# Kernel optimization log

Hardware: AMD Instinct MI355X
Metric: run time of the kernel (lower is better)

## Reference

```python
import jax, jax.numpy as jnp
import numpy as np

B, C, H, W, K = 16, 64, 256, 256, 3

def setup_inputs() -> dict:
    key = jax.random.key(0)
    ks = jax.random.split(key, 3)
    x = jax.random.normal(ks[0], (B, C, H, W), dtype=jnp.float32)
    # ReDistribution params
    rd_k = jnp.ones((1, C, 1, 1), jnp.float32)
    rd_b = jnp.zeros((1, C, 1, 1), jnp.float32)
    # Spectral binary activation beta
    beta = jnp.ones((1,), jnp.float32)
    # HardBinaryConv real-valued latent weights (Conv2d default init scale)
    fan_in = C * K * K
    bound = 1.0 / np.sqrt(fan_in)
    conv_w = jax.random.uniform(ks[1], (C, C, K, K), jnp.float32, -bound, bound)
    # RPReLU params
    pr_bias0 = jnp.zeros((1, C, 1, 1), jnp.float32)
    prelu_w = jnp.full((C,), 0.25, jnp.float32)
    pr_bias1 = jnp.zeros((1, C, 1, 1), jnp.float32)
    return {"x": x, "rd_k": rd_k, "rd_b": rd_b, "beta": beta,
            "conv_w": conv_w, "pr_bias0": pr_bias0, "prelu_w": prelu_w,
            "pr_bias1": pr_bias1}

def _ste(hard, soft):
    # straight-through estimator: forward=hard, backward grads flow via soft
    return jax.lax.stop_gradient(hard - soft) + soft

def reference(x, rd_k, rd_b, beta, conv_w, pr_bias0, prelu_w, pr_bias1):
    sg = jax.lax.stop_gradient
    # ReDistribution
    out = x * rd_k + rd_b
    # Spectral binary activation with tanh STE
    out = _ste(jnp.sign(out), jnp.tanh(out * beta))
    # HardBinaryConv: per-output-channel mean |w| scaling, sign binarize, clip STE
    scaling = sg(jnp.mean(jnp.abs(conv_w), axis=(1, 2, 3), keepdims=True))  # [C,1,1,1]
    bw = _ste(scaling * jnp.sign(conv_w), jnp.clip(conv_w, -1.0, 1.0))
    y = jax.lax.conv_general_dilated(
        out, bw, window_strides=(1, 1), padding=((1, 1), (1, 1)),
        dimension_numbers=("NCHW", "OIHW", "NCHW"))
    # RPReLU: bias0 -> per-channel PReLU -> bias1
    y = y + pr_bias0
    y = jnp.where(y >= 0, y, prelu_w[None, :, None, None] * y)
    y = y + pr_bias1
    return y + x
```

## Files before the change

kernel.cpp:

```cpp
#include <hip/hip_runtime.h>
#include <cstdint>
#include <cstddef>

#define Bn 16
#define Cn 64
#define Hn 256
#define Wn 256
#define HWn (Hn * Wn)
#define TH 8
#define ROWS (TH + 2)
#define COLS (Wn + 2)
#define NBLK (Bn * (Hn / TH))

typedef unsigned long long u64;
typedef u64   u64x2 __attribute__((ext_vector_type(2)));
typedef float f32x4 __attribute__((ext_vector_type(4)));

__global__ __launch_bounds__(64) void pack_weights(const float* __restrict__ w,
                                                   const float* __restrict__ b0g,
                                                   const float* __restrict__ pwg,
                                                   const float* __restrict__ b1g,
                                                   u64* __restrict__ wbits,
                                                   float4* __restrict__ par,
                                                   int* __restrict__ corrx) {
    const int co = blockIdx.x;
    const int ci = threadIdx.x;
    const float* wp = w + ((size_t)co * Cn + ci) * 9;
    float v[9];
    float asum = 0.f;
    #pragma unroll
    for (int t = 0; t < 9; ++t) { v[t] = wp[t]; asum += fabsf(v[t]); }
    u64 m[9];
    #pragma unroll
    for (int t = 0; t < 9; ++t) m[t] = __ballot(v[t] > 0.f);
    #pragma unroll
    for (int off = 32; off; off >>= 1) asum += __shfl_xor(asum, off);
    if (ci == 0) {
        int c[9];
        #pragma unroll
        for (int t = 0; t < 9; ++t) {
            wbits[co * 9 + t] = m[t];
            c[t] = 64 - 2 * (int)__popcll(m[t]);
        }
        int* cx = corrx + co * 8;
        cx[0] = c[0] + c[1] + c[2];
        cx[1] = c[6] + c[7] + c[8];
        cx[2] = c[0] + c[3] + c[6];
        cx[3] = c[2] + c[5] + c[8];
        cx[4] = c[0]; cx[5] = c[2];
        cx[6] = c[6]; cx[7] = c[8];
        par[co] = make_float4(asum * (1.f / (Cn * 9)), b0g[co], pwg[co], b1g[co]);
    }
}

__global__ __launch_bounds__(256, 3) void fused(const float* __restrict__ x,
                                                const float* __restrict__ rdk,
                                                const float* __restrict__ rdb,
                                                const u64* __restrict__ wbits,
                                                const float4* __restrict__ par,
                                                const int* __restrict__ corrx,
                                                float* __restrict__ out,
                                                int clobber) {
    __shared__ __align__(16) u64 s_a[ROWS][COLS];
    __shared__ float2 s_rd[Cn];

    const int tid = threadIdx.x;
    const int bid     = blockIdx.x;
    const int logical = (bid & 7) * (NBLK / 8) + (bid >> 3);
    const int n  = logical >> 5;
    const int h0 = (logical & 31) * TH;

    if (tid < Cn) s_rd[tid] = make_float2(rdk[tid], rdb[tid]);
    if (tid < 2 * ROWS) s_a[tid >> 1][(tid & 1) ? (COLS - 1) : 0] = 0;
    __syncthreads();

    const float* xn = x + (size_t)n * Cn * HWn;
    #pragma unroll
    for (int it = 0; it < 5; ++it) {
        const int task = tid + it * 256;
        const int r  = task >> 7;
        const int c  = (task & 127) * 2;
        const int gh = h0 - 1 + r;
        u64 b0 = 0, b1 = 0;
        if (gh >= 0 && gh < Hn) {
            const float* xp = xn + (size_t)gh * Wn + c;
            #pragma unroll 8
            for (int ci = 0; ci < Cn; ++ci) {
                const float2 kb = s_rd[ci];
                const float2 v = *reinterpret_cast<const float2*>(xp + (size_t)ci * HWn);
                const u64 bit = 1ull << ci;
                if (fmaf(v.x, kb.x, kb.y) > 0.f) b0 |= bit;
                if (fmaf(v.y, kb.x, kb.y) > 0.f) b1 |= bit;
            }
        }
        s_a[r][1 + c] = b0;
        s_a[r][2 + c] = b1;
    }
    __syncthreads();

    const int r  = tid >> 5;
    const int c0 = (tid & 31) * 8;

    u64 A[3][10];
    #pragma unroll
    for (int dh = 0; dh < 3; ++dh)
        #pragma unroll
        for (int q = 0; q < 5; ++q) {
            const u64x2 t = *reinterpret_cast<const u64x2*>(&s_a[r + dh][c0 + 2 * q]);
            A[dh][2 * q]     = t.x;
            A[dh][2 * q + 1] = t.y;
        }
    if (clobber) s_a[0][tid] = 0;

    const int htop = (h0 == 0) & (r == 0);
    const int hbot = (h0 + TH == Hn) & (r == TH - 1);
    const int wl = (c0 == 0), wr = (c0 == Wn - 8);
    const int need = htop | hbot | wl | wr;
    const int h = h0 + r;

    const float* xp = x   + (size_t)n * Cn * HWn + (size_t)h * Wn + c0;
    float*       op = out + (size_t)n * Cn * HWn + (size_t)h * Wn + c0;

    f32x4 xa = *reinterpret_cast<const f32x4*>(xp);
    f32x4 xb = *reinterpret_cast<const f32x4*>(xp + 4);
    #pragma unroll 2
    for (int co = 0; co < Cn; ++co) {
        const int nco = (co < Cn - 1) ? co + 1 : co;
        const f32x4 xa_n = *reinterpret_cast<const f32x4*>(xp + (size_t)nco * HWn);
        const f32x4 xb_n = *reinterpret_cast<const f32x4*>(xp + (size_t)nco * HWn + 4);

        const u64* wb = wbits + co * 9;
        int isum[8];
        #pragma unroll
        for (int p = 0; p < 8; ++p) {
            int acc = 0;
            #pragma unroll
            for (int dh = 0; dh < 3; ++dh) {
                acc += (int)__popcll(A[dh][p]     ^ wb[dh * 3]);
                acc += (int)__popcll(A[dh][p + 1] ^ wb[dh * 3 + 1]);
                acc += (int)__popcll(A[dh][p + 2] ^ wb[dh * 3 + 2]);
            }
            isum[p] = 576 - 2 * acc;
        }

        if (need) {
            const int* cx = corrx + co * 8;
            const int sb = (htop ? cx[0] : 0) + (hbot ? cx[1] : 0);
            #pragma unroll
            for (int p = 0; p < 8; ++p) isum[p] -= sb;
            if (wl) isum[0] -= cx[2] - (htop ? cx[4] : 0) - (hbot ? cx[6] : 0);
            if (wr) isum[7] -= cx[3] - (htop ? cx[5] : 0) - (hbot ? cx[7] : 0);
        }

        const float4 p4 = par[co];
        f32x4 o0, o1;
        #pragma unroll
        for (int j = 0; j < 4; ++j) {
            float y = fmaf(p4.x, (float)isum[j], p4.y);
            y = (y >= 0.f) ? y : y * p4.z;
            o0[j] = y + p4.w + xa[j];
        }
        #pragma unroll
        for (int j = 0; j < 4; ++j) {
            float y = fmaf(p4.x, (float)isum[4 + j], p4.y);
            y = (y >= 0.f) ? y : y * p4.z;
            o1[j] = y + p4.w + xb[j];
        }
        __builtin_nontemporal_store(o0, reinterpret_cast<f32x4*>(op + (size_t)co * HWn));
        __builtin_nontemporal_store(o1, reinterpret_cast<f32x4*>(op + (size_t)co * HWn + 4));
        xa = xa_n;
        xb = xb_n;
    }
}

extern "C" void kernel_launch(void* const* d_in, const int* in_sizes, int n_in,
                              void* d_out, int out_size, void* d_ws, size_t ws_size,
                              hipStream_t stream) {
    const float* x      = (const float*)d_in[0];
    const float* rd_k   = (const float*)d_in[1];
    const float* rd_b   = (const float*)d_in[2];
    const float* conv_w = (const float*)d_in[4];
    const float* pb0    = (const float*)d_in[5];
    const float* pw     = (const float*)d_in[6];
    const float* pb1    = (const float*)d_in[7];
    float* out = (float*)d_out;

    uint8_t* ws = (uint8_t*)d_ws;
    u64*    wbits = (u64*)ws;
    float4* par   = (float4*)(ws + 4608);
    int*    corrx = (int*)(ws + 4608 + 1024);

    pack_weights<<<Cn, 64, 0, stream>>>(conv_w, pb0, pw, pb1, wbits, par, corrx);
    fused<<<NBLK, 256, 0, stream>>>(x, rd_k, rd_b, wbits, par, corrx, out, 0);
}
```

Baseline: 159.9 us.

## Split image rows into half-width tiles with halo columns and LDS-cached params

Each block now covers an 8-row by 128-column tile instead of a full 256-wide row strip, so the grid doubles and each thread emits 4 outputs instead of 8. Halo columns at tile edges are binarized separately, which adds redundant loads of x at every tile boundary. The per-channel epilogue parameters are staged into reused shared memory instead of being read from global each iteration. The aim is more parallelism and lower register pressure, at the cost of extra halo work and an extra barrier.

New measurement: 161.5 us. About the same (+1.1%).

```diff
diff --git a/kernel.cpp b/kernel.cpp
--- a/kernel.cpp
+++ b/kernel.cpp
@@ -8,9 +8,10 @@
 #define Wn 256
 #define HWn (Hn * Wn)
 #define TH 8
+#define TW 128
 #define ROWS (TH + 2)
-#define COLS (Wn + 2)
-#define NBLK (Bn * (Hn / TH))
+#define COLS (TW + 2)
+#define NBLK (Bn * (Hn / TH) * (Wn / TW))
 
 typedef unsigned long long u64;
 typedef u64   u64x2 __attribute__((ext_vector_type(2)));
@@ -53,86 +54,106 @@
     }
 }
 
-__global__ __launch_bounds__(256, 3) void fused(const float* __restrict__ x,
-                                                const float* __restrict__ rdk,
-                                                const float* __restrict__ rdb,
-                                                const u64* __restrict__ wbits,
-                                                const float4* __restrict__ par,
-                                                const int* __restrict__ corrx,
-                                                float* __restrict__ out,
-                                                int clobber) {
+__global__ __launch_bounds__(256) void fused(const float* __restrict__ x,
+                                             const float* __restrict__ rdk,
+                                             const float* __restrict__ rdb,
+                                             const u64* __restrict__ wbits,
+                                             const float4* __restrict__ par,
+                                             const int* __restrict__ corrx,
+                                             float* __restrict__ out) {
     __shared__ __align__(16) u64 s_a[ROWS][COLS];
     __shared__ float2 s_rd[Cn];
 
     const int tid = threadIdx.x;
     const int bid     = blockIdx.x;
     const int logical = (bid & 7) * (NBLK / 8) + (bid >> 3);
-    const int n  = logical >> 5;
-    const int h0 = (logical & 31) * TH;
+    const int n   = logical >> 6;
+    const int rem = logical & 63;
+    const int h0  = (rem >> 1) * TH;
+    const int w0  = (rem & 1) * TW;
 
     if (tid < Cn) s_rd[tid] = make_float2(rdk[tid], rdb[tid]);
-    if (tid < 2 * ROWS) s_a[tid >> 1][(tid & 1) ? (COLS - 1) : 0] = 0;
     __syncthreads();
 
     const float* xn = x + (size_t)n * Cn * HWn;
     #pragma unroll
-    for (int it = 0; it < 5; ++it) {
+    for (int it = 0; it < 3; ++it) {
         const int task = tid + it * 256;
-        const int r  = task >> 7;
-        const int c  = (task & 127) * 2;
-        const int gh = h0 - 1 + r;
-        u64 b0 = 0, b1 = 0;
-        if (gh >= 0 && gh < Hn) {
-            const float* xp = xn + (size_t)gh * Wn + c;
-            #pragma unroll 8
-            for (int ci = 0; ci < Cn; ++ci) {
-                const float2 kb = s_rd[ci];
-                const float2 v = *reinterpret_cast<const float2*>(xp + (size_t)ci * HWn);
-                const u64 bit = 1ull << ci;
-                if (fmaf(v.x, kb.x, kb.y) > 0.f) b0 |= bit;
-                if (fmaf(v.y, kb.x, kb.y) > 0.f) b1 |= bit;
+        if (task < 640) {
+            const int r = task >> 6;
+            const int k = task & 63;
+            const int gh = h0 - 1 + r;
+            const int gw = w0 + 2 * k;
+            u64 b0 = 0, b1 = 0;
+            if (gh >= 0 && gh < Hn) {
+                const float* xp = xn + (size_t)gh * Wn + gw;
+                #pragma unroll 8
+                for (int ci = 0; ci < Cn; ++ci) {
+                    const float2 kb = s_rd[ci];
+                    const float2 v = *reinterpret_cast<const float2*>(xp + (size_t)ci * HWn);
+                    const u64 bit = 1ull << ci;
+                    if (fmaf(v.x, kb.x, kb.y) > 0.f) b0 |= bit;
+                    if (fmaf(v.y, kb.x, kb.y) > 0.f) b1 |= bit;
+                }
             }
-        }
-        s_a[r][1 + c] = b0;
-        s_a[r][2 + c] = b1;
+            s_a[r][1 + 2 * k] = b0;
+            s_a[r][2 + 2 * k] = b1;
+        } else if (task < 660) {
+            const int t2 = task - 640;
+            const int r = t2 >> 1;
+            const int side = t2 & 1;
+            const int gh = h0 - 1 + r;
+            const int gw = side ? (w0 + TW) : (w0 - 1);
+            u64 b = 0;
+            if (gh >= 0 && gh < Hn && gw >= 0 && gw < Wn) {
+                const float* xp = xn + (size_t)gh * Wn + gw;
+                #pragma unroll 8
+                for (int ci = 0; ci < Cn; ++ci) {
+                    const float2 kb = s_rd[ci];
+                    if (fmaf(xp[(size_t)ci * HWn], kb.x, kb.y) > 0.f) b |= 1ull << ci;
+                }
+            }
+            s_a[r][side ? (COLS - 1) : 0] = b;
+        }
     }
     __syncthreads();
 
     const int r  = tid >> 5;
-    const int c0 = (tid & 31) * 8;
-
-    u64 A[3][10];
+    const int c0 = (tid & 31) * 4;
+
+    u64 A[3][6];
     #pragma unroll
     for (int dh = 0; dh < 3; ++dh)
         #pragma unroll
-        for (int q = 0; q < 5; ++q) {
+        for (int q = 0; q < 3; ++q) {
             const u64x2 t = *reinterpret_cast<const u64x2*>(&s_a[r + dh][c0 + 2 * q]);
             A[dh][2 * q]     = t.x;
             A[dh][2 * q + 1] = t.y;
         }
-    if (clobber) s_a[0][tid] = 0;
-
-    const int htop = (h0 == 0) & (r == 0);
-    const int hbot = (h0 + TH == Hn) & (r == TH - 1);
-    const int wl = (c0 == 0), wr = (c0 == Wn - 8);
+    __syncthreads();
+    float4* parL = reinterpret_cast<float4*>(&s_a[0][0]);
+    if (tid < Cn) parL[tid] = par[tid];
+    __syncthreads();
+
+    const int gw0  = w0 + c0;
+    const int h    = h0 + r;
+    const int htop = (h == 0), hbot = (h == Hn - 1);
+    const int wl   = (gw0 == 0), wr = (gw0 + 3 == Wn - 1);
     const int need = htop | hbot | wl | wr;
-    const int h = h0 + r;
-
-    const float* xp = x   + (size_t)n * Cn * HWn + (size_t)h * Wn + c0;
-    float*       op = out + (size_t)n * Cn * HWn + (size_t)h * Wn + c0;
+
+    const float* xp = x   + (size_t)n * Cn * HWn + (size_t)h * Wn + gw0;
+    float*       op = out + (size_t)n * Cn * HWn + (size_t)h * Wn + gw0;
 
     f32x4 xa = *reinterpret_cast<const f32x4*>(xp);
-    f32x4 xb = *reinterpret_cast<const f32x4*>(xp + 4);
     #pragma unroll 2
     for (int co = 0; co < Cn; ++co) {
         const int nco = (co < Cn - 1) ? co + 1 : co;
         const f32x4 xa_n = *reinterpret_cast<const f32x4*>(xp + (size_t)nco * HWn);
-        const f32x4 xb_n = *reinterpret_cast<const f32x4*>(xp + (size_t)nco * HWn + 4);
 
         const u64* wb = wbits + co * 9;
-        int isum[8];
-        #pragma unroll
-        for (int p = 0; p < 8; ++p) {
+        int isum[4];
+        #pragma unroll
+        for (int p = 0; p < 4; ++p) {
             int acc = 0;
             #pragma unroll
             for (int dh = 0; dh < 3; ++dh) {
@@ -147,29 +168,21 @@
             const int* cx = corrx + co * 8;
             const int sb = (htop ? cx[0] : 0) + (hbot ? cx[1] : 0);
             #pragma unroll
-            for (int p = 0; p < 8; ++p) isum[p] -= sb;
+            for (int p = 0; p < 4; ++p) isum[p] -= sb;
             if (wl) isum[0] -= cx[2] - (htop ? cx[4] : 0) - (hbot ? cx[6] : 0);
-            if (wr) isum[7] -= cx[3] - (htop ? cx[5] : 0) - (hbot ? cx[7] : 0);
-        }
-
-        const float4 p4 = par[co];
-        f32x4 o0, o1;
+            if (wr) isum[3] -= cx[3] - (htop ? cx[5] : 0) - (hbot ? cx[7] : 0);
+        }
+
+        const float4 p4 = parL[co];
+        f32x4 o;
         #pragma unroll
         for (int j = 0; j < 4; ++j) {
             float y = fmaf(p4.x, (float)isum[j], p4.y);
             y = (y >= 0.f) ? y : y * p4.z;
-            o0[j] = y + p4.w + xa[j];
-        }
-        #pragma unroll
-        for (int j = 0; j < 4; ++j) {
-            float y = fmaf(p4.x, (float)isum[4 + j], p4.y);
-            y = (y >= 0.f) ? y : y * p4.z;
-            o1[j] = y + p4.w + xb[j];
-        }
-        __builtin_nontemporal_store(o0, reinterpret_cast<f32x4*>(op + (size_t)co * HWn));
-        __builtin_nontemporal_store(o1, reinterpret_cast<f32x4*>(op + (size_t)co * HWn + 4));
+            o[j] = y + p4.w + xa[j];
+        }
+        __builtin_nontemporal_store(o, reinterpret_cast<f32x4*>(op + (size_t)co * HWn));
         xa = xa_n;
-        xb = xb_n;
     }
 }
 
@@ -191,5 +204,5 @@
     int*    corrx = (int*)(ws + 4608 + 1024);
 
     pack_weights<<<Cn, 64, 0, stream>>>(conv_w, pb0, pw, pb1, wbits, par, corrx);
-    fused<<<NBLK, 256, 0, stream>>>(x, rd_k, rd_b, wbits, par, corrx, out, 0);
+    fused<<<NBLK, 256, 0, stream>>>(x, rd_k, rd_b, wbits, par, corrx, out);
 }
```
